# Optimization experiments

Hardware: AMD Instinct MI355X
Metric: run time of the kernel (lower is better)

Reference implementation:

```python
import jax, jax.numpy as jnp
import numpy as np

NUM_NODES = 100000
EMBED_DIM = 128
HIDDEN = 128
NUM_EDGES = 1600000


def gcn_conv(x, W, b, src, dst, num_nodes):
    """PyG GCNConv: x' = D^{-1/2} (A+I) D^{-1/2} (x W) + b, symmetric norm with self-loops."""
    x = x @ W  # [N, out]
    loops = jnp.arange(num_nodes, dtype=src.dtype)
    s = jnp.concatenate([src, loops])  # sources incl. self-loops
    d = jnp.concatenate([dst, loops])  # targets incl. self-loops
    deg = jax.ops.segment_sum(jnp.ones_like(d, dtype=x.dtype), d, num_segments=num_nodes)
    dis = jnp.where(deg > 0, jax.lax.rsqrt(deg), 0.0)  # deg^{-1/2}, 0 where isolated
    norm = dis[s] * dis[d]  # [E+N]
    msg = x[s] * norm[:, None]  # gather + scale
    out = jax.ops.segment_sum(msg, d, num_segments=num_nodes)  # scatter-add
    return out + b


def setup_inputs() -> dict:
    key = jax.random.key(0)
    k1, k2, k3, k4, k5, k6 = jax.random.split(key, 6)
    edge_index = jax.random.randint(k1, (2, NUM_EDGES), 0, NUM_NODES, dtype=jnp.int64)
    edge_attr = jax.random.normal(k2, (NUM_EDGES,), dtype=jnp.float32)
    emb = jax.random.normal(k3, (NUM_NODES, EMBED_DIM), dtype=jnp.float32) * 0.1
    W1 = jax.random.normal(k4, (EMBED_DIM, HIDDEN), dtype=jnp.float32) * (1.0 / np.sqrt(EMBED_DIM))
    b1 = jnp.zeros((HIDDEN,), dtype=jnp.float32)
    W2 = jax.random.normal(k5, (HIDDEN, HIDDEN), dtype=jnp.float32) * (1.0 / np.sqrt(HIDDEN))
    b2 = jnp.zeros((HIDDEN,), dtype=jnp.float32)
    return {"edge_index": edge_index, "edge_attr": edge_attr, "emb": emb,
            "W1": W1, "b1": b1, "W2": W2, "b2": b2}


def reference(edge_index, edge_attr, emb, W1, b1, W2, b2):
    src, dst = edge_index[0], edge_index[1]
    x = gcn_conv(emb, W1, b1, src, dst, NUM_NODES)
    x = jax.nn.relu(x)
    x = gcn_conv(x, W2, b2, src, dst, NUM_NODES)
    return x
```

## Files before the change

### kernel.cpp

```cpp
#include <hip/hip_runtime.h>

#define EMB 128
#define NBUC 1024
#define NPART 256
#define PREPB 128

typedef __attribute__((ext_vector_type(8))) short short8;
typedef __attribute__((ext_vector_type(4))) float f32x4;

__device__ __forceinline__ unsigned short f2bf(float f) {
    union { float f; unsigned int i; } v; v.f = f;
    unsigned int x = v.i;
    x += 0x7fffu + ((x >> 16) & 1u);
    return (unsigned short)(x >> 16);
}
__device__ __forceinline__ void acc_fma4(uint2 v, float d,
                                         float& a0, float& a1, float& a2, float& a3) {
    union { unsigned int i; float f; } t;
    t.i = v.x << 16;          a0 = fmaf(d, t.f, a0);
    t.i = v.x & 0xffff0000u;  a1 = fmaf(d, t.f, a1);
    t.i = v.y << 16;          a2 = fmaf(d, t.f, a2);
    t.i = v.y & 0xffff0000u;  a3 = fmaf(d, t.f, a3);
}
__device__ __forceinline__ void acc_bf4(uint2 v,
                                        float& a0, float& a1, float& a2, float& a3) {
    union { unsigned int i; float f; } t;
    t.i = v.x << 16;          a0 += t.f;
    t.i = v.x & 0xffff0000u;  a1 += t.f;
    t.i = v.y << 16;          a2 += t.f;
    t.i = v.y & 0xffff0000u;  a3 += t.f;
}


__device__ __forceinline__ void p1_body(int bid, int* h, const int* __restrict__ dst,
                                        int* __restrict__ tot, int E, int chunk) {
    for (int i = threadIdx.x; i < NBUC; i += 256) h[i] = 0;
    __syncthreads();
    int s = bid * chunk;
    int e = min(E, s + chunk);
    for (int i = s + threadIdx.x; i < e; i += 256)
        atomicAdd(&h[dst[i] >> 7], 1);
    __syncthreads();
    for (int i = threadIdx.x; i < NBUC; i += 256) {
        int v = h[i];
        if (v) atomicAdd(&tot[i], v);
    }
}

__device__ __forceinline__ void prepw_body(int bid, const float* __restrict__ W1,
                                           const float* __restrict__ W2,
                                           unsigned short* __restrict__ W1s,
                                           unsigned short* __restrict__ W2s) {
    int gid = bid * 256 + threadIdx.x;
    const float* W = (gid < 16384) ? W1 : W2;
    unsigned short* Ws = (gid < 16384) ? W1s : W2s;
    int idx = gid & 16383;
    int k = idx >> 7, n = idx & 127;
    int kk = k >> 5, q = (k >> 3) & 3, j = k & 7;
    int ct = n >> 4, nn = n & 15;
    int didx = ((((kk * 8 + ct) * 4 + q) * 16 + nn) << 3) + j;
    Ws[didx] = f2bf(W[idx]);
}

__global__ __launch_bounds__(256) void k_start(const int* __restrict__ dst,
                                               int* __restrict__ tot, int E, int chunk,
                                               const float* __restrict__ W1,
                                               const float* __restrict__ W2,
                                               unsigned short* __restrict__ W1s,
                                               unsigned short* __restrict__ W2s) {
    __shared__ int h[NBUC];
    int b = blockIdx.x;
    if (b < NPART) p1_body(b, h, dst, tot, E, chunk);
    else           prepw_body(b - NPART, W1, W2, W1s, W2s);
}

__global__ __launch_bounds__(1024) void p_scan(const int* __restrict__ tot,
                                               int* __restrict__ base,
                                               int* __restrict__ gcnt, int E) {
    __shared__ int a[NBUC];
    int t = threadIdx.x;
    int v0 = tot[t];
    a[t] = v0;
    __syncthreads();
    for (int off = 1; off < NBUC; off <<= 1) {
        int v = (t >= off) ? a[t - off] : 0;
        __syncthreads();
        a[t] += v;
        __syncthreads();
    }
    int excl = a[t] - v0;
    base[t] = excl;
    gcnt[t] = excl;
    if (t == NBUC - 1) base[NBUC] = E;
}

__device__ __forceinline__ void scatter_body(int bid, int* cnt,
                                             const int* __restrict__ src,
                                             const int* __restrict__ dst,
                                             int* __restrict__ gcnt,
                                             int* __restrict__ part,
                                             int E, int chunk) {
    for (int i = threadIdx.x; i < NBUC; i += 256) cnt[i] = 0;
    __syncthreads();
    int s = bid * chunk;
    int e = min(E, s + chunk);
    for (int i = s + threadIdx.x; i < e; i += 256)
        atomicAdd(&cnt[dst[i] >> 7], 1);
    __syncthreads();
    for (int i = threadIdx.x; i < NBUC; i += 256) {
        int c = cnt[i];
        cnt[i] = c ? atomicAdd(&gcnt[i], c) : 0;
    }
    __syncthreads();
    for (int i = s + threadIdx.x; i < e; i += 256) {
        int d = dst[i];
        int pos = atomicAdd(&cnt[d >> 7], 1);
        part[pos] = src[i] | ((d & 127) << 17);
    }
}

__global__ __launch_bounds__(256) void p3_csr(const int* __restrict__ part,
                                              const int* __restrict__ base,
                                              int* __restrict__ R, int* __restrict__ adj,
                                              float* __restrict__ dis, int N, int E) {
    __shared__ int hist[128];
    __shared__ int sc[128];
    __shared__ int cnt[128];
    int b = blockIdx.x;
    int n0 = b * 128;
    int nn = min(128, N - n0);
    int s = base[b], e = base[b + 1];
    int t = threadIdx.x;

    if (t < 128) hist[t] = 0;
    __syncthreads();
    for (int i = s + t; i < e; i += 256)
        atomicAdd(&hist[part[i] >> 17], 1);
    __syncthreads();

    if (t < 128) sc[t] = hist[t];
    __syncthreads();
    for (int off = 1; off < 128; off <<= 1) {
        int v = 0;
        if (t < 128 && t >= off) v = sc[t - off];
        __syncthreads();
        if (t < 128) sc[t] += v;
        __syncthreads();
    }
    if (t < 128) {
        int excl = sc[t] - hist[t];
        cnt[t] = excl;
        if (t < nn) {
            R[n0 + t] = s + excl;
            dis[n0 + t] = rsqrtf((float)hist[t] + 1.0f);
        }
    }
    if (b == 0 && t == 0) R[N] = E;
    __syncthreads();

    for (int i = s + t; i < e; i += 256) {
        int p = part[i];
        int pos = atomicAdd(&cnt[p >> 17], 1);
        adj[s + pos] = p & 0x1FFFF;
    }
}

template <bool XBF16, bool SCALE>
__device__ __forceinline__ void gemm_body(int bid, unsigned short* lds,
    const void* Xv, const unsigned short* __restrict__ Wsw,
    const float* __restrict__ dis, unsigned short* __restrict__ Y, int N)
{
    {
        const uint4* srcp = (const uint4*)Wsw;
        uint4* dstp = (uint4*)lds;
        for (int i = threadIdx.x; i < 2048; i += 256) dstp[i] = srcp[i];
    }
    __syncthreads();

    const int wave = threadIdx.x >> 6;
    const int lane = threadIdx.x & 63;
    const int q = lane >> 4, nn = lane & 15;
    const int row0 = bid * 64 + wave * 16;
    const int arow = row0 + nn;
    const int arc = arow < N ? arow : N - 1;

    f32x4 acc[8];
#pragma unroll
    for (int ct = 0; ct < 8; ++ct) acc[ct] = (f32x4){0.f, 0.f, 0.f, 0.f};

#pragma unroll
    for (int kk = 0; kk < 4; ++kk) {
        short8 af;
        if (XBF16) {
            af = *(const short8*)((const unsigned short*)Xv + (size_t)arc * EMB + kk * 32 + q * 8);
        } else {
            const float* xp = (const float*)Xv + (size_t)arc * EMB + kk * 32 + q * 8;
            float4 u0 = *(const float4*)xp;
            float4 u1 = *(const float4*)(xp + 4);
            af[0] = (short)f2bf(u0.x); af[1] = (short)f2bf(u0.y);
            af[2] = (short)f2bf(u0.z); af[3] = (short)f2bf(u0.w);
            af[4] = (short)f2bf(u1.x); af[5] = (short)f2bf(u1.y);
            af[6] = (short)f2bf(u1.z); af[7] = (short)f2bf(u1.w);
        }
#pragma unroll
        for (int ct = 0; ct < 8; ++ct) {
            short8 bf = ((const short8*)lds)[(kk * 8 + ct) * 64 + lane];
            acc[ct] = __builtin_amdgcn_mfma_f32_16x16x32_bf16(af, bf, acc[ct], 0, 0, 0);
        }
    }

    __syncthreads();

    float dv[4];
    if (SCALE) {
#pragma unroll
        for (int r = 0; r < 4; ++r) {
            int gm = row0 + q * 4 + r;
            dv[r] = dis[gm < N ? gm : N - 1];
        }
    }
#pragma unroll
    for (int ct = 0; ct < 8; ++ct) {
#pragma unroll
        for (int r = 0; r < 4; ++r) {
            int ml = wave * 16 + q * 4 + r;
            float val = SCALE ? acc[ct][r] * dv[r] : acc[ct][r];
            lds[ml * 136 + ct * 16 + nn] = f2bf(val);
        }
    }
    __syncthreads();

    const int rbase = bid * 64;
    for (int i = threadIdx.x; i < 1024; i += 256) {
        int row = i >> 4, off = i & 15;
        int grow = rbase + row;
        if (grow < N) {
            uint4 v = *(const uint4*)(lds + row * 136 + off * 8);
            *((uint4*)(Y + (size_t)grow * EMB) + off) = v;
        }
    }
}

__global__ __launch_bounds__(256) void k_mid(
    const int* __restrict__ src, const int* __restrict__ dstp,
    int* __restrict__ gcnt, int* __restrict__ part, int E, int chunk,
    const void* Xv, const unsigned short* __restrict__ W1s,
    unsigned short* __restrict__ Y, int N)
{
    __shared__ __align__(16) unsigned short smem[16384];
    int b = blockIdx.x;
    if (b < NPART) scatter_body(b, (int*)smem, src, dstp, gcnt, part, E, chunk);
    else           gemm_body<false, false>(b - NPART, smem, Xv, W1s, nullptr, Y, N);
}

__global__ __launch_bounds__(256) void k_gemm2(
    const void* Xv, const unsigned short* __restrict__ Wsw,
    const float* __restrict__ dis, unsigned short* __restrict__ Y, int N)
{
    __shared__ __align__(16) unsigned short smem[16384];
    gemm_body<true, true>(blockIdx.x, smem, Xv, Wsw, dis, Y, N);
}

template <bool FOLD, bool RELU, bool BF16OUT>
__global__ __launch_bounds__(256) void k_gather_finalize(
    const int* __restrict__ R, const int* __restrict__ adj,
    const unsigned short* __restrict__ Y, const float* __restrict__ dis,
    const float* __restrict__ bias, void* __restrict__ Outv, int N)
{
    int t = blockIdx.x * 256 + threadIdx.x;
    int n = t >> 5;
    if (n >= N) return;
    int j = (t & 31) * 4;

    int rs = R[n], re = R[n + 1];
    float dv = dis[n];

    float a0 = 0.f, a1 = 0.f, a2 = 0.f, a3 = 0.f;
    uint2 sv = *(const uint2*)(Y + (size_t)n * EMB + j);
    if (FOLD) acc_fma4(sv, dv, a0, a1, a2, a3);
    else      acc_bf4(sv, a0, a1, a2, a3);

    int e = rs;
    for (; e + 7 < re; e += 8) {
        int s0 = adj[e],     s1 = adj[e + 1], s2 = adj[e + 2], s3 = adj[e + 3];
        int s4 = adj[e + 4], s5 = adj[e + 5], s6 = adj[e + 6], s7 = adj[e + 7];
        uint2 v0 = *(const uint2*)(Y + (size_t)s0 * EMB + j);
        uint2 v1 = *(const uint2*)(Y + (size_t)s1 * EMB + j);
        uint2 v2 = *(const uint2*)(Y + (size_t)s2 * EMB + j);
        uint2 v3 = *(const uint2*)(Y + (size_t)s3 * EMB + j);
        uint2 v4 = *(const uint2*)(Y + (size_t)s4 * EMB + j);
        uint2 v5 = *(const uint2*)(Y + (size_t)s5 * EMB + j);
        uint2 v6 = *(const uint2*)(Y + (size_t)s6 * EMB + j);
        uint2 v7 = *(const uint2*)(Y + (size_t)s7 * EMB + j);
        if (FOLD) {
            float d0 = dis[s0], d1 = dis[s1], d2 = dis[s2], d3 = dis[s3];
            float d4 = dis[s4], d5 = dis[s5], d6 = dis[s6], d7 = dis[s7];
            acc_fma4(v0, d0, a0, a1, a2, a3); acc_fma4(v1, d1, a0, a1, a2, a3);
            acc_fma4(v2, d2, a0, a1, a2, a3); acc_fma4(v3, d3, a0, a1, a2, a3);
            acc_fma4(v4, d4, a0, a1, a2, a3); acc_fma4(v5, d5, a0, a1, a2, a3);
            acc_fma4(v6, d6, a0, a1, a2, a3); acc_fma4(v7, d7, a0, a1, a2, a3);
        } else {
            acc_bf4(v0, a0, a1, a2, a3); acc_bf4(v1, a0, a1, a2, a3);
            acc_bf4(v2, a0, a1, a2, a3); acc_bf4(v3, a0, a1, a2, a3);
            acc_bf4(v4, a0, a1, a2, a3); acc_bf4(v5, a0, a1, a2, a3);
            acc_bf4(v6, a0, a1, a2, a3); acc_bf4(v7, a0, a1, a2, a3);
        }
    }
    for (; e + 3 < re; e += 4) {
        int s0 = adj[e], s1 = adj[e + 1], s2 = adj[e + 2], s3 = adj[e + 3];
        uint2 v0 = *(const uint2*)(Y + (size_t)s0 * EMB + j);
        uint2 v1 = *(const uint2*)(Y + (size_t)s1 * EMB + j);
        uint2 v2 = *(const uint2*)(Y + (size_t)s2 * EMB + j);
        uint2 v3 = *(const uint2*)(Y + (size_t)s3 * EMB + j);
        if (FOLD) {
            float d0 = dis[s0], d1 = dis[s1], d2 = dis[s2], d3 = dis[s3];
            acc_fma4(v0, d0, a0, a1, a2, a3); acc_fma4(v1, d1, a0, a1, a2, a3);
            acc_fma4(v2, d2, a0, a1, a2, a3); acc_fma4(v3, d3, a0, a1, a2, a3);
        } else {
            acc_bf4(v0, a0, a1, a2, a3); acc_bf4(v1, a0, a1, a2, a3);
            acc_bf4(v2, a0, a1, a2, a3); acc_bf4(v3, a0, a1, a2, a3);
        }
    }
    for (; e < re; ++e) {
        int s0 = adj[e];
        uint2 v0 = *(const uint2*)(Y + (size_t)s0 * EMB + j);
        if (FOLD) acc_fma4(v0, dis[s0], a0, a1, a2, a3);
        else      acc_bf4(v0, a0, a1, a2, a3);
    }

    float4 b = *(const float4*)(bias + j);
    float o0 = dv * a0 + b.x;
    float o1 = dv * a1 + b.y;
    float o2 = dv * a2 + b.z;
    float o3 = dv * a3 + b.w;
    if (RELU) {
        o0 = fmaxf(o0, 0.f); o1 = fmaxf(o1, 0.f);
        o2 = fmaxf(o2, 0.f); o3 = fmaxf(o3, 0.f);
    }
    if (BF16OUT) {
        ushort4 o = { f2bf(o0), f2bf(o1), f2bf(o2), f2bf(o3) };
        *(ushort4*)((unsigned short*)Outv + (size_t)n * EMB + j) = o;
    } else {
        float4 o = { o0, o1, o2, o3 };
        *(float4*)((float*)Outv + (size_t)n * EMB + j) = o;
    }
}

extern "C" void kernel_launch(void* const* d_in, const int* in_sizes, int n_in,
                              void* d_out, int out_size, void* d_ws, size_t ws_size,
                              hipStream_t stream) {
    const int* ei = (const int*)d_in[0];
    const int E = in_sizes[0] / 2;
    const float* emb = (const float*)d_in[2];
    const int N = in_sizes[2] / EMB;
    const float* W1 = (const float*)d_in[3];
    const float* b1 = (const float*)d_in[4];
    const float* W2 = (const float*)d_in[5];
    const float* b2 = (const float*)d_in[6];
    float* out = (float*)d_out;

    const int* src = ei;
    const int* dstp = ei + E;

    char* w = (char*)d_ws;
    auto take = [&](size_t bytes) { char* p = w; w += (bytes + 511) & ~(size_t)511; return p; };
    float* dis  = (float*)take((size_t)N * 4);
    int*   R    = (int*)  take((size_t)(N + 1) * 4);
    int*   base = (int*)  take((size_t)(NBUC + 1) * 4);
    int*   tot  = (int*)  take((size_t)NBUC * 4);
    int*   gcnt = (int*)  take((size_t)NBUC * 4);
    int*   adj  = (int*)  take((size_t)E * 4);
    unsigned short* W1s = (unsigned short*)take((size_t)EMB * EMB * 2);
    unsigned short* W2s = (unsigned short*)take((size_t)EMB * EMB * 2);
    unsigned short* Hb  = (unsigned short*)take((size_t)N * EMB * 2);
    int*   part = (int*)Hb;
    unsigned short* Y1b = (unsigned short*)d_out;

    const int NB = (N + 127) / 128;
    const int chunk = (E + NPART - 1) / NPART;
    const int gM = (N + 63) / 64;
    const int gG = (N * 32 + 255) / 256;

    hipMemsetAsync(tot, 0, (size_t)NBUC * 4, stream);

    k_start<<<NPART + PREPB, 256, 0, stream>>>(dstp, tot, E, chunk, W1, W2, W1s, W2s);

    p_scan<<<1, NBUC, 0, stream>>>(tot, base, gcnt, E);

    k_mid<<<NPART + gM, 256, 0, stream>>>(src, dstp, gcnt, part, E, chunk,
                                          emb, W1s, Y1b, N);

    p3_csr<<<NB, 256, 0, stream>>>(part, base, R, adj, dis, N, E);

    k_gather_finalize<true, true, true><<<gG, 256, 0, stream>>>(R, adj, Y1b, dis, b1, Hb, N);

    k_gemm2<<<gM, 256, 0, stream>>>(Hb, W2s, dis, Hb, N);
    k_gather_finalize<false, false, false><<<gG, 256, 0, stream>>>(R, adj, Hb, dis, b2, out, N);
}
```

Before: 327.6 us.

## Split gather into two column-half passes and drop 8-way unroll

The gather/finalize kernel now processes each node's 128 features as two 64-column halves handled by separate block ranges. The first half of the grid does columns 0-63 and the second half does 64-127, with 16 threads per node instead of 32. This shrinks the gathered working set per pass, so the randomly accessed Y rows may stay in cache better. In exchange, adjacency indices and dis are read twice, and removing the 8-wide unrolled loop lowers memory-level parallelism per thread.

Measured after the change: 325.6 us. About the same (-0.6%).

```diff
diff --git a/kernel.cpp b/kernel.cpp
--- a/kernel.cpp
+++ b/kernel.cpp
@@ -262,15 +262,17 @@
 }
 
 template <bool FOLD, bool RELU, bool BF16OUT>
-__global__ __launch_bounds__(256) void k_gather_finalize(
+__global__ __launch_bounds__(256) void k_gather_split(
     const int* __restrict__ R, const int* __restrict__ adj,
     const unsigned short* __restrict__ Y, const float* __restrict__ dis,
-    const float* __restrict__ bias, void* __restrict__ Outv, int N)
+    const float* __restrict__ bias, void* __restrict__ Outv, int N, int half)
 {
-    int t = blockIdx.x * 256 + threadIdx.x;
-    int n = t >> 5;
+    int bid = blockIdx.x;
+    int pass = (bid >= half) ? 1 : 0;
+    int t = (bid - pass * half) * 256 + threadIdx.x;
+    int n = t >> 4;
     if (n >= N) return;
-    int j = (t & 31) * 4;
+    int j = pass * 64 + (t & 15) * 4;
 
     int rs = R[n], re = R[n + 1];
     float dv = dis[n];
@@ -281,31 +283,6 @@
     else      acc_bf4(sv, a0, a1, a2, a3);
 
     int e = rs;
-    for (; e + 7 < re; e += 8) {
-        int s0 = adj[e],     s1 = adj[e + 1], s2 = adj[e + 2], s3 = adj[e + 3];
-        int s4 = adj[e + 4], s5 = adj[e + 5], s6 = adj[e + 6], s7 = adj[e + 7];
-        uint2 v0 = *(const uint2*)(Y + (size_t)s0 * EMB + j);
-        uint2 v1 = *(const uint2*)(Y + (size_t)s1 * EMB + j);
-        uint2 v2 = *(const uint2*)(Y + (size_t)s2 * EMB + j);
-        uint2 v3 = *(const uint2*)(Y + (size_t)s3 * EMB + j);
-        uint2 v4 = *(const uint2*)(Y + (size_t)s4 * EMB + j);
-        uint2 v5 = *(const uint2*)(Y + (size_t)s5 * EMB + j);
-        uint2 v6 = *(const uint2*)(Y + (size_t)s6 * EMB + j);
-        uint2 v7 = *(const uint2*)(Y + (size_t)s7 * EMB + j);
-        if (FOLD) {
-            float d0 = dis[s0], d1 = dis[s1], d2 = dis[s2], d3 = dis[s3];
-            float d4 = dis[s4], d5 = dis[s5], d6 = dis[s6], d7 = dis[s7];
-            acc_fma4(v0, d0, a0, a1, a2, a3); acc_fma4(v1, d1, a0, a1, a2, a3);
-            acc_fma4(v2, d2, a0, a1, a2, a3); acc_fma4(v3, d3, a0, a1, a2, a3);
-            acc_fma4(v4, d4, a0, a1, a2, a3); acc_fma4(v5, d5, a0, a1, a2, a3);
-            acc_fma4(v6, d6, a0, a1, a2, a3); acc_fma4(v7, d7, a0, a1, a2, a3);
-        } else {
-            acc_bf4(v0, a0, a1, a2, a3); acc_bf4(v1, a0, a1, a2, a3);
-            acc_bf4(v2, a0, a1, a2, a3); acc_bf4(v3, a0, a1, a2, a3);
-            acc_bf4(v4, a0, a1, a2, a3); acc_bf4(v5, a0, a1, a2, a3);
-            acc_bf4(v6, a0, a1, a2, a3); acc_bf4(v7, a0, a1, a2, a3);
-        }
-    }
     for (; e + 3 < re; e += 4) {
         int s0 = adj[e], s1 = adj[e + 1], s2 = adj[e + 2], s3 = adj[e + 3];
         uint2 v0 = *(const uint2*)(Y + (size_t)s0 * EMB + j);
@@ -379,7 +356,8 @@
     const int NB = (N + 127) / 128;
     const int chunk = (E + NPART - 1) / NPART;
     const int gM = (N + 63) / 64;
-    const int gG = (N * 32 + 255) / 256;
+    const int half = (N * 16 + 255) / 256;
+    const int gG = 2 * half;
 
     hipMemsetAsync(tot, 0, (size_t)NBUC * 4, stream);
 
@@ -392,8 +370,8 @@
 
     p3_csr<<<NB, 256, 0, stream>>>(part, base, R, adj, dis, N, E);
 
-    k_gather_finalize<true, true, true><<<gG, 256, 0, stream>>>(R, adj, Y1b, dis, b1, Hb, N);
+    k_gather_split<true, true, true><<<gG, 256, 0, stream>>>(R, adj, Y1b, dis, b1, Hb, N, half);
 
     k_gemm2<<<gM, 256, 0, stream>>>(Hb, W2s, dis, Hb, N);
-    k_gather_finalize<false, false, false><<<gG, 256, 0, stream>>>(R, adj, Hb, dis, b2, out, N);
-}
+    k_gather_split<false, false, false><<<gG, 256, 0, stream>>>(R, adj, Hb, dis, b2, out, N, half);
+}
```
